# Kernel tuning notes

Measured on AMD Instinct MI355X. Metric: run time of the kernel, lower is better.

Reference implementation:

```python
import jax, jax.numpy as jnp
import numpy as np

B = 65536      # batch of (state, action) pairs
DIM_S = 64     # input feature dim
DIM_C = 8      # number of options / experts
H = 256        # hidden width (two hidden layers)


def setup_inputs() -> dict:
    key = jax.random.key(0)
    ks = jax.random.split(key, 7)
    s = 0.05  # small init scale
    st = jax.random.normal(ks[0], (B, DIM_S), dtype=jnp.float32)
    # Batched expert weights: one slice per expert (dim_c experts).
    W1 = jax.random.normal(ks[1], (DIM_C, DIM_S, H), dtype=jnp.float32) * s
    b1 = jax.random.normal(ks[2], (DIM_C, H), dtype=jnp.float32) * s
    W2 = jax.random.normal(ks[3], (DIM_C, H, H), dtype=jnp.float32) * s
    b2 = jax.random.normal(ks[4], (DIM_C, H), dtype=jnp.float32) * s
    W3 = jax.random.normal(ks[5], (DIM_C, H, 1), dtype=jnp.float32) * s
    b3 = jax.random.normal(ks[6], (DIM_C, 1), dtype=jnp.float32) * s
    return {"st": st, "W1": W1, "b1": b1, "W2": W2, "b2": b2,
            "W3": W3, "b3": b3}


def reference(st, W1, b1, W2, b2, W3, b3):
    # Equivalent of torch.stack([m(st) for m in self.discriminator], dim=1):
    # every expert MLP (dim_s -> H -> H -> 1, ReLU) applied to the same st,
    # expressed as batched GEMMs over the expert axis c.
    h = jax.nn.relu(jnp.einsum('bs,csh->bch', st, W1) + b1[None])   # [B, C, H]
    h = jax.nn.relu(jnp.einsum('bch,chk->bck', h, W2) + b2[None])   # [B, C, H]
    d = jnp.einsum('bch,cho->bco', h, W3) + b3[None]                # [B, C, 1]
    return d
```

## Files before the change

kernel.cpp:

```cpp
#include <hip/hip_runtime.h>
#include <hip/hip_bf16.h>

typedef __bf16 bf16x8 __attribute__((ext_vector_type(8)));
typedef float  f32x4  __attribute__((ext_vector_type(4)));

static constexpr int S  = 64;
static constexpr int C  = 8;
static constexpr int HD = 256;

__device__ __forceinline__ unsigned short f2bf(float f) {
  __hip_bfloat16 b = __float2bfloat16(f);
  unsigned short u;
  __builtin_memcpy(&u, &b, 2);
  return u;
}

__device__ __forceinline__ void gl2lds16(const void* g, void* l) {
  __builtin_amdgcn_global_load_lds(
      (const __attribute__((address_space(1))) unsigned int*)g,
      (__attribute__((address_space(3))) unsigned int*)l, 16, 0, 0);
}

__global__ __launch_bounds__(256) void prep_weights(
    const float* __restrict__ W1, const float* __restrict__ W2,
    unsigned short* __restrict__ W1T, unsigned short* __restrict__ W2T)
{
  __shared__ float tile[32][33];
  const int tid = threadIdx.x, cl = tid & 31, r0 = tid >> 5;
  const int b = blockIdx.x;
  if (b < 512) {
    const int c = b >> 6, t = b & 63, kt = t >> 3, nt = t & 7;
    const float* src = W2 + c * 65536;
    #pragma unroll
    for (int i = 0; i < 4; ++i) {
      int r = r0 + 8 * i;
      tile[r][cl] = src[(kt * 32 + r) * 256 + nt * 32 + cl];
    }
    __syncthreads();
    unsigned short* dst = W2T + c * 65536;
    #pragma unroll
    for (int i = 0; i < 4; ++i) {
      int r = r0 + 8 * i;
      dst[(nt * 32 + r) * 256 + kt * 32 + cl] = f2bf(tile[cl][r]);
    }
  } else {
    const int bb = b - 512;
    const int c = bb >> 4, t = bb & 15, st2 = t >> 3, ht = t & 7;
    const float* src = W1 + c * 16384;
    #pragma unroll
    for (int i = 0; i < 4; ++i) {
      int r = r0 + 8 * i;
      tile[r][cl] = src[(st2 * 32 + r) * 256 + ht * 32 + cl];
    }
    __syncthreads();
    unsigned short* dst = W1T + c * 16384;
    #pragma unroll
    for (int i = 0; i < 4; ++i) {
      int r = r0 + 8 * i;
      dst[(ht * 32 + r) * 64 + st2 * 32 + cl] = f2bf(tile[cl][r]);
    }
  }
}

__global__ __launch_bounds__(256, 2) void moe_fused(
    const float* __restrict__ st,
    const unsigned short* __restrict__ W1T,
    const unsigned short* __restrict__ W2T,
    const float* __restrict__ b1,
    const float* __restrict__ b2,
    const float* __restrict__ W3,
    const float* __restrict__ b3,
    float* __restrict__ out)
{
  constexpr int LDT = 72;

  __shared__ __align__(16) unsigned short sT[256 * LDT];
  __shared__ __align__(16) unsigned short sW2[2 * 32 * 256];

  const int tid  = threadIdx.x;
  const int lane = tid & 63;
  const int wv   = tid >> 6;
  const int l15  = lane & 15;
  const int q    = lane >> 4;
  const int c    = blockIdx.x >> 8;
  const int row0 = (blockIdx.x & 255) * 256;

  const unsigned short* W1c = W1T + c * HD * S;
  const unsigned short* W2c = W2T + c * HD * HD;

  bf16x8 aA[4][2];
  #pragma unroll
  for (int rt = 0; rt < 4; ++rt)
    #pragma unroll
    for (int ks = 0; ks < 2; ++ks) {
      const int row = row0 + wv * 64 + rt * 16 + l15;
      const float4* p = reinterpret_cast<const float4*>(st + (size_t)row * S + ks * 32 + q * 8);
      float4 x = p[0], y = p[1];
      union { bf16x8 v; unsigned short u[8]; } a;
      a.u[0] = f2bf(x.x); a.u[1] = f2bf(x.y); a.u[2] = f2bf(x.z); a.u[3] = f2bf(x.w);
      a.u[4] = f2bf(y.x); a.u[5] = f2bf(y.y); a.u[6] = f2bf(y.z); a.u[7] = f2bf(y.w);
      aA[rt][ks] = a.v;
    }

  float pb1[4][4];
  #pragma unroll
  for (int cc = 0; cc < 4; ++cc)
    #pragma unroll
    for (int ctl = 0; ctl < 4; ++ctl)
      pb1[cc][ctl] = b1[c * HD + (cc * 4 + ctl) * 16 + l15];
  float pb2[8][2], pw3[8][2];
  #pragma unroll
  for (int ch = 0; ch < 8; ++ch)
    #pragma unroll
    for (int ct = 0; ct < 2; ++ct) {
      const int n = ch * 32 + ct * 16 + l15;
      pb2[ch][ct] = b2[c * HD + n];
      pw3[ch][ct] = W3[c * HD + n];
    }
  const float bb3 = b3[c];

  bf16x8 aF[4][4][2];
  bool dma_started = false;
  #pragma unroll
  for (int cc = 0; cc < 4; ++cc) {
    f32x4 acc[4][4];
    #pragma unroll
    for (int rt = 0; rt < 4; ++rt)
      #pragma unroll
      for (int ctl = 0; ctl < 4; ++ctl)
        acc[rt][ctl] = (f32x4){0.f, 0.f, 0.f, 0.f};

    #pragma unroll
    for (int ks = 0; ks < 2; ++ks) {
      const int koff = ks * 32 + q * 8;
      bf16x8 bq[4];
      #pragma unroll
      for (int ctl = 0; ctl < 4; ++ctl)
        bq[ctl] = *reinterpret_cast<const bf16x8*>(
            W1c + ((cc * 4 + ctl) * 16 + l15) * S + koff);

      if (cc == 0 && ks == 0 && !dma_started) {
        dma_started = true;
        #pragma unroll
        for (int pc = 0; pc < 2; ++pc) {
          unsigned short* buf = sW2 + pc * (32 * 256);
          #pragma unroll
          for (int i = 0; i < 4; ++i) {
            const int b2i = wv * 4 + i;
            const int r   = b2i * 2 + (lane >> 5);
            const int p   = lane & 31;
            const int j   = p ^ (r & 7);
            gl2lds16(W2c + (pc * 32 + r) * 256 + j * 8, buf + b2i * 512);
          }
        }
      }

      #pragma unroll
      for (int ctl = 0; ctl < 4; ++ctl)
        #pragma unroll
        for (int rt = 0; rt < 4; ++rt)
          acc[rt][ctl] = __builtin_amdgcn_mfma_f32_16x16x32_bf16(
              aA[rt][ks], bq[ctl], acc[rt][ctl], 0, 0, 0);
    }

    #pragma unroll
    for (int rt = 0; rt < 4; ++rt) {
      const int rbase = wv * 64 + rt * 16 + q * 4;
      #pragma unroll
      for (int ctl = 0; ctl < 4; ++ctl) {
        const float bias = pb1[cc][ctl];
        #pragma unroll
        for (int r = 0; r < 4; ++r) {
          float v = acc[rt][ctl][r] + bias;
          v = v > 0.f ? v : 0.f;
          sT[(rbase + r) * LDT + ctl * 16 + l15] = f2bf(v);
        }
      }
    }
    __asm__ __volatile__("s_waitcnt lgkmcnt(0)" ::: "memory");
    #pragma unroll
    for (int rt = 0; rt < 4; ++rt)
      #pragma unroll
      for (int k2 = 0; k2 < 2; ++k2)
        aF[cc][rt][k2] = *reinterpret_cast<const bf16x8*>(
            sT + (wv * 64 + rt * 16 + l15) * LDT + k2 * 32 + q * 8);
    __asm__ __volatile__("s_waitcnt lgkmcnt(0)" ::: "memory");
  }

  __syncthreads();

  float dacc[4][4];
  #pragma unroll
  for (int rt = 0; rt < 4; ++rt)
    #pragma unroll
    for (int r = 0; r < 4; ++r) dacc[rt][r] = 0.f;

  #pragma unroll
  for (int ch = 0; ch < 8; ++ch) {
    const unsigned short* buf = sW2 + (ch & 1) * (32 * 256);

    f32x4 acc[4][2];
    #pragma unroll
    for (int rt = 0; rt < 4; ++rt)
      #pragma unroll
      for (int ct = 0; ct < 2; ++ct)
        acc[rt][ct] = (f32x4){0.f, 0.f, 0.f, 0.f};

    #pragma unroll
    for (int ks = 0; ks < 8; ++ks) {
      const int jj = ks * 4 + q;
      const int cc = ks >> 1, k2 = ks & 1;
      #pragma unroll
      for (int ct = 0; ct < 2; ++ct) {
        const int nl = ct * 16 + l15;
        bf16x8 b = *reinterpret_cast<const bf16x8*>(
            buf + nl * 256 + ((jj ^ (l15 & 7)) << 3));
        #pragma unroll
        for (int rt = 0; rt < 4; ++rt)
          acc[rt][ct] = __builtin_amdgcn_mfma_f32_16x16x32_bf16(
              aF[cc][rt][k2], b, acc[rt][ct], 0, 0, 0);
      }
    }

    #pragma unroll
    for (int ct = 0; ct < 2; ++ct) {
      const float bias = pb2[ch][ct];
      const float w3v  = pw3[ch][ct];
      #pragma unroll
      for (int rt = 0; rt < 4; ++rt)
        #pragma unroll
        for (int r = 0; r < 4; ++r) {
          float v = acc[rt][ct][r] + bias;
          v = v > 0.f ? v : 0.f;
          dacc[rt][r] += v * w3v;
        }
    }

    __syncthreads();
    if (ch < 6) {
      unsigned short* nbuf = sW2 + (ch & 1) * (32 * 256);
      #pragma unroll
      for (int i = 0; i < 4; ++i) {
        const int b2i = wv * 4 + i;
        const int r   = b2i * 2 + (lane >> 5);
        const int p   = lane & 31;
        const int j   = p ^ (r & 7);
        gl2lds16(W2c + ((ch + 2) * 32 + r) * 256 + j * 8, nbuf + b2i * 512);
      }
    }
  }

  #pragma unroll
  for (int rt = 0; rt < 4; ++rt)
    #pragma unroll
    for (int r = 0; r < 4; ++r) {
      float v = dacc[rt][r];
      v += __shfl_xor(v, 1);
      v += __shfl_xor(v, 2);
      v += __shfl_xor(v, 4);
      v += __shfl_xor(v, 8);
      dacc[rt][r] = v;
    }

  if (l15 == 0) {
    const int rbase = row0 + wv * 64 + q * 4;
    #pragma unroll
    for (int rt = 0; rt < 4; ++rt)
      #pragma unroll
      for (int r = 0; r < 4; ++r)
        out[(rbase + rt * 16 + r) * C + c] = dacc[rt][r] + bb3;
  }
}

extern "C" void kernel_launch(void* const* d_in, const int* in_sizes, int n_in,
                              void* d_out, int out_size, void* d_ws, size_t ws_size,
                              hipStream_t stream)
{
  const float* st = (const float*)d_in[0];
  const float* W1 = (const float*)d_in[1];
  const float* b1 = (const float*)d_in[2];
  const float* W2 = (const float*)d_in[3];
  const float* b2 = (const float*)d_in[4];
  const float* W3 = (const float*)d_in[5];
  const float* b3 = (const float*)d_in[6];
  float* out = (float*)d_out;

  unsigned short* W1T = (unsigned short*)d_ws;
  unsigned short* W2T = W1T + C * HD * S;

  prep_weights<<<dim3(640), dim3(256), 0, stream>>>(W1, W2, W1T, W2T);
  moe_fused<<<dim3(2048), dim3(256), 0, stream>>>(st, W1T, W2T, b1, b2, W3, b3, out);
}
```

Before: 180.5 us.

## Drop LDS staging of W2, read weights directly from global/L2

Removes the double-buffered global_load_lds staging of W2 and its per-chunk block barriers, and instead has each wave load W2 B-fragments straight from global memory (relying on L2/L1 caching since all blocks of an expert share the same weights). Layer 1 is transposed so W1 is the A operand, letting bias loads become vector loads and hidden activations be written to LDS as packed 4-wide stores. Bias and W3 preloads are moved into the chunk loop with partial unrolling to cut register pressure. The trade is more redundant global/L1 traffic per wave and exposed load latency in place of LDS reuse and synchronization.

Measured after the change: 241.2 us. 33.6% more time.

```diff
diff --git a/kernel.cpp b/kernel.cpp
--- a/kernel.cpp
+++ b/kernel.cpp
@@ -13,12 +13,6 @@
   unsigned short u;
   __builtin_memcpy(&u, &b, 2);
   return u;
-}
-
-__device__ __forceinline__ void gl2lds16(const void* g, void* l) {
-  __builtin_amdgcn_global_load_lds(
-      (const __attribute__((address_space(1))) unsigned int*)g,
-      (__attribute__((address_space(3))) unsigned int*)l, 16, 0, 0);
 }
 
 __global__ __launch_bounds__(256) void prep_weights(
@@ -75,7 +69,6 @@
   constexpr int LDT = 72;
 
   __shared__ __align__(16) unsigned short sT[256 * LDT];
-  __shared__ __align__(16) unsigned short sW2[2 * 32 * 256];
 
   const int tid  = threadIdx.x;
   const int lane = tid & 63;
@@ -90,91 +83,58 @@
 
   bf16x8 aA[4][2];
   #pragma unroll
-  for (int rt = 0; rt < 4; ++rt)
+  for (int nt = 0; nt < 4; ++nt)
     #pragma unroll
     for (int ks = 0; ks < 2; ++ks) {
-      const int row = row0 + wv * 64 + rt * 16 + l15;
+      const int row = row0 + wv * 64 + nt * 16 + l15;
       const float4* p = reinterpret_cast<const float4*>(st + (size_t)row * S + ks * 32 + q * 8);
       float4 x = p[0], y = p[1];
       union { bf16x8 v; unsigned short u[8]; } a;
       a.u[0] = f2bf(x.x); a.u[1] = f2bf(x.y); a.u[2] = f2bf(x.z); a.u[3] = f2bf(x.w);
       a.u[4] = f2bf(y.x); a.u[5] = f2bf(y.y); a.u[6] = f2bf(y.z); a.u[7] = f2bf(y.w);
-      aA[rt][ks] = a.v;
-    }
-
-  float pb1[4][4];
-  #pragma unroll
-  for (int cc = 0; cc < 4; ++cc)
-    #pragma unroll
-    for (int ctl = 0; ctl < 4; ++ctl)
-      pb1[cc][ctl] = b1[c * HD + (cc * 4 + ctl) * 16 + l15];
-  float pb2[8][2], pw3[8][2];
-  #pragma unroll
-  for (int ch = 0; ch < 8; ++ch)
-    #pragma unroll
-    for (int ct = 0; ct < 2; ++ct) {
-      const int n = ch * 32 + ct * 16 + l15;
-      pb2[ch][ct] = b2[c * HD + n];
-      pw3[ch][ct] = W3[c * HD + n];
-    }
-  const float bb3 = b3[c];
+      aA[nt][ks] = a.v;
+    }
 
   bf16x8 aF[4][4][2];
-  bool dma_started = false;
   #pragma unroll
   for (int cc = 0; cc < 4; ++cc) {
     f32x4 acc[4][4];
     #pragma unroll
-    for (int rt = 0; rt < 4; ++rt)
-      #pragma unroll
-      for (int ctl = 0; ctl < 4; ++ctl)
-        acc[rt][ctl] = (f32x4){0.f, 0.f, 0.f, 0.f};
+    for (int mt = 0; mt < 4; ++mt)
+      #pragma unroll
+      for (int nt = 0; nt < 4; ++nt)
+        acc[mt][nt] = (f32x4){0.f, 0.f, 0.f, 0.f};
 
     #pragma unroll
     for (int ks = 0; ks < 2; ++ks) {
       const int koff = ks * 32 + q * 8;
-      bf16x8 bq[4];
-      #pragma unroll
-      for (int ctl = 0; ctl < 4; ++ctl)
-        bq[ctl] = *reinterpret_cast<const bf16x8*>(
-            W1c + ((cc * 4 + ctl) * 16 + l15) * S + koff);
-
-      if (cc == 0 && ks == 0 && !dma_started) {
-        dma_started = true;
+      bf16x8 aW[4];
+      #pragma unroll
+      for (int mt = 0; mt < 4; ++mt)
+        aW[mt] = *reinterpret_cast<const bf16x8*>(
+            W1c + (cc * 64 + mt * 16 + l15) * S + koff);
+      #pragma unroll
+      for (int mt = 0; mt < 4; ++mt)
         #pragma unroll
-        for (int pc = 0; pc < 2; ++pc) {
-          unsigned short* buf = sW2 + pc * (32 * 256);
-          #pragma unroll
-          for (int i = 0; i < 4; ++i) {
-            const int b2i = wv * 4 + i;
-            const int r   = b2i * 2 + (lane >> 5);
-            const int p   = lane & 31;
-            const int j   = p ^ (r & 7);
-            gl2lds16(W2c + (pc * 32 + r) * 256 + j * 8, buf + b2i * 512);
-          }
-        }
-      }
-
-      #pragma unroll
-      for (int ctl = 0; ctl < 4; ++ctl)
-        #pragma unroll
-        for (int rt = 0; rt < 4; ++rt)
-          acc[rt][ctl] = __builtin_amdgcn_mfma_f32_16x16x32_bf16(
-              aA[rt][ks], bq[ctl], acc[rt][ctl], 0, 0, 0);
-    }
-
-    #pragma unroll
-    for (int rt = 0; rt < 4; ++rt) {
-      const int rbase = wv * 64 + rt * 16 + q * 4;
-      #pragma unroll
-      for (int ctl = 0; ctl < 4; ++ctl) {
-        const float bias = pb1[cc][ctl];
-        #pragma unroll
-        for (int r = 0; r < 4; ++r) {
-          float v = acc[rt][ctl][r] + bias;
-          v = v > 0.f ? v : 0.f;
-          sT[(rbase + r) * LDT + ctl * 16 + l15] = f2bf(v);
-        }
+        for (int nt = 0; nt < 4; ++nt)
+          acc[mt][nt] = __builtin_amdgcn_mfma_f32_16x16x32_bf16(
+              aW[mt], aA[nt][ks], acc[mt][nt], 0, 0, 0);
+    }
+
+    #pragma unroll
+    for (int mt = 0; mt < 4; ++mt) {
+      const f32x4 bias = *reinterpret_cast<const f32x4*>(
+          b1 + c * HD + cc * 64 + mt * 16 + q * 4);
+      #pragma unroll
+      for (int nt = 0; nt < 4; ++nt) {
+        ushort4 pk;
+        float v0 = acc[mt][nt][0] + bias[0]; v0 = v0 > 0.f ? v0 : 0.f;
+        float v1 = acc[mt][nt][1] + bias[1]; v1 = v1 > 0.f ? v1 : 0.f;
+        float v2 = acc[mt][nt][2] + bias[2]; v2 = v2 > 0.f ? v2 : 0.f;
+        float v3 = acc[mt][nt][3] + bias[3]; v3 = v3 > 0.f ? v3 : 0.f;
+        pk.x = f2bf(v0); pk.y = f2bf(v1); pk.z = f2bf(v2); pk.w = f2bf(v3);
+        *reinterpret_cast<ushort4*>(
+            sT + (wv * 64 + nt * 16 + l15) * LDT + mt * 16 + q * 4) = pk;
       }
     }
     __asm__ __volatile__("s_waitcnt lgkmcnt(0)" ::: "memory");
@@ -187,17 +147,21 @@
     __asm__ __volatile__("s_waitcnt lgkmcnt(0)" ::: "memory");
   }
 
-  __syncthreads();
-
   float dacc[4][4];
   #pragma unroll
   for (int rt = 0; rt < 4; ++rt)
     #pragma unroll
     for (int r = 0; r < 4; ++r) dacc[rt][r] = 0.f;
 
-  #pragma unroll
+  #pragma unroll 2
   for (int ch = 0; ch < 8; ++ch) {
-    const unsigned short* buf = sW2 + (ch & 1) * (32 * 256);
+    float pb2v[2], pw3v[2];
+    #pragma unroll
+    for (int ct = 0; ct < 2; ++ct) {
+      const int n = ch * 32 + ct * 16 + l15;
+      pb2v[ct] = b2[c * HD + n];
+      pw3v[ct] = W3[c * HD + n];
+    }
 
     f32x4 acc[4][2];
     #pragma unroll
@@ -208,24 +172,23 @@
 
     #pragma unroll
     for (int ks = 0; ks < 8; ++ks) {
-      const int jj = ks * 4 + q;
+      const int koff = ks * 32 + q * 8;
       const int cc = ks >> 1, k2 = ks & 1;
       #pragma unroll
       for (int ct = 0; ct < 2; ++ct) {
-        const int nl = ct * 16 + l15;
-        bf16x8 b = *reinterpret_cast<const bf16x8*>(
-            buf + nl * 256 + ((jj ^ (l15 & 7)) << 3));
+        bf16x8 bW = *reinterpret_cast<const bf16x8*>(
+            W2c + (ch * 32 + ct * 16 + l15) * HD + koff);
         #pragma unroll
         for (int rt = 0; rt < 4; ++rt)
           acc[rt][ct] = __builtin_amdgcn_mfma_f32_16x16x32_bf16(
-              aF[cc][rt][k2], b, acc[rt][ct], 0, 0, 0);
+              aF[cc][rt][k2], bW, acc[rt][ct], 0, 0, 0);
       }
     }
 
     #pragma unroll
     for (int ct = 0; ct < 2; ++ct) {
-      const float bias = pb2[ch][ct];
-      const float w3v  = pw3[ch][ct];
+      const float bias = pb2v[ct];
+      const float w3v  = pw3v[ct];
       #pragma unroll
       for (int rt = 0; rt < 4; ++rt)
         #pragma unroll
@@ -235,19 +198,6 @@
           dacc[rt][r] += v * w3v;
         }
     }
-
-    __syncthreads();
-    if (ch < 6) {
-      unsigned short* nbuf = sW2 + (ch & 1) * (32 * 256);
-      #pragma unroll
-      for (int i = 0; i < 4; ++i) {
-        const int b2i = wv * 4 + i;
-        const int r   = b2i * 2 + (lane >> 5);
-        const int p   = lane & 31;
-        const int j   = p ^ (r & 7);
-        gl2lds16(W2c + ((ch + 2) * 32 + r) * 256 + j * 8, nbuf + b2i * 512);
-      }
-    }
   }
 
   #pragma unroll
@@ -263,6 +213,7 @@
     }
 
   if (l15 == 0) {
+    const float bb3 = b3[c];
     const int rbase = row0 + wv * 64 + q * 4;
     #pragma unroll
     for (int rt = 0; rt < 4; ++rt)
```
